# Kernel tuning notes

Measured on AMD Instinct MI355X. Metric: run time of the kernel, lower is better.

The kernel has to match this reference:

```python
import jax, jax.numpy as jnp
import numpy as np

B = 2048

def _conv(x, w, b, stride):
    y = jax.lax.conv_general_dilated(x, w, (stride, stride), 'VALID',
                                     dimension_numbers=('NCHW', 'OIHW', 'NCHW'))
    return y + b[None, :, None, None]

def _local_conv(x, w, b):
    # w: (Ho, Wo, Co, Ci, kh, kw), b: (Ho, Wo, Co); stride 1, valid
    Ho, Wo, Co, Ci, kh, kw = w.shape
    # patches: (B, Ci, kh*kw, Ho, Wo) -- sliding windows, small fixed loop over kernel taps
    patches = jnp.stack([x[:, :, i:i + Ho, j:j + Wo]
                         for i in range(kh) for j in range(kw)], axis=2)
    wf = w.reshape(Ho, Wo, Co, Ci, kh * kw)
    y = jnp.einsum('bcphw,hwocp->bohw', patches, wf)
    return y + jnp.transpose(b, (2, 0, 1))[None]

def setup_inputs() -> dict:
    key = jax.random.key(0)
    ks = jax.random.split(key, 18)
    s = 0.05
    inp = {
        'x': jax.random.normal(ks[0], (B, 5, 60, 60), dtype=jnp.float32),
        'info': jax.random.normal(ks[1], (B, 8), dtype=jnp.float32),
        'w1': jax.random.normal(ks[2], (32, 5, 3, 3), dtype=jnp.float32) * s,
        'b1': jnp.zeros((32,), dtype=jnp.float32),
        'w2a': jax.random.normal(ks[3], (64, 32, 3, 3), dtype=jnp.float32) * s,
        'b2a': jnp.zeros((64,), dtype=jnp.float32),
        'w2b': jax.random.normal(ks[4], (64, 64, 3, 3), dtype=jnp.float32) * s,
        'b2b': jnp.zeros((64,), dtype=jnp.float32),
        'lw3': jax.random.normal(ks[5], (9, 9, 64, 64, 5, 5), dtype=jnp.float32) * s,
        'lb3': jnp.zeros((9, 9, 64), dtype=jnp.float32),
        'lw4': jax.random.normal(ks[6], (5, 5, 64, 64, 5, 5), dtype=jnp.float32) * s,
        'lb4': jnp.zeros((5, 5, 64), dtype=jnp.float32),
        'lw5': jax.random.normal(ks[7], (3, 3, 64, 64, 3, 3), dtype=jnp.float32) * s,
        'lb5': jnp.zeros((3, 3, 64), dtype=jnp.float32),
        'hw': jax.random.normal(ks[8], (2, 584), dtype=jnp.float32) * s,
        'hb': jnp.zeros((2,), dtype=jnp.float32),
    }
    return inp

def reference(x, info, w1, b1, w2a, b2a, w2b, b2b, lw3, lb3, lw4, lb4, lw5, lb5, hw, hb):
    h = jnp.tanh(_conv(x, w1, b1, 2))            # (B,32,29,29)
    h = jnp.tanh(_conv(h, w2a, b2a, 1))          # (B,64,27,27)
    h = jnp.tanh(_conv(h, w2b, b2b, 2))          # (B,64,13,13)
    h = jnp.tanh(_local_conv(h, lw3, lb3))       # (B,64,9,9)
    h = jnp.tanh(_local_conv(h, lw4, lb4))       # (B,64,5,5)
    h = jnp.tanh(_local_conv(h, lw5, lb5))       # (B,64,3,3)
    h = h.reshape(h.shape[0], -1)                # (B,576)
    h = jnp.concatenate([h, info], axis=1)       # (B,584)
    logits = h @ hw.T + hb                       # (B,2)
    return jax.nn.softmax(logits, axis=1)
```

## Files before the change

### kernel.cpp

```cpp
#include <hip/hip_runtime.h>
#include <stdint.h>

#define THREADS 256

typedef short bf16x8 __attribute__((ext_vector_type(8)));
typedef float f32x4 __attribute__((ext_vector_type(4)));
typedef unsigned uint2_ __attribute__((ext_vector_type(2)));

#define GPTR(x) ((const __attribute__((address_space(1))) void*)(x))
#define LPTR(x) ((__attribute__((address_space(3))) void*)(x))

__device__ __forceinline__ unsigned short f2bf(float v) {
  unsigned u = __builtin_bit_cast(unsigned, v);
  u = (u + 0x7fff + ((u >> 16) & 1)) >> 16;
  return (unsigned short)u;
}
__device__ __forceinline__ float bf2f(unsigned short h) {
  return __builtin_bit_cast(float, (unsigned)h << 16);
}
__device__ __forceinline__ float fast_tanh(float x) {
  return 1.f - 2.f / (__expf(2.f * x) + 1.f);
}

__device__ __forceinline__ int xcd_swizzle(int wg, int nwg) {
  const int q = nwg >> 3, rr = nwg & 7;
  const int xcd = wg & 7, l = wg >> 3;
  return (xcd < rr ? xcd * (q + 1) : rr * (q + 1) + (xcd - rr) * q) + l;
}

__global__ void pack_w1t(const float* __restrict__ w1, float* __restrict__ w1t) {
  int idx = blockIdx.x * THREADS + threadIdx.x;
  if (idx >= 45 * 32) return;
  int t = idx >> 5, co = idx & 31;
  w1t[t * 32 + co] = w1[co * 45 + t];
}

__global__ void __launch_bounds__(256) conv1_direct(
    const float* __restrict__ x, const float* __restrict__ w1t,
    const float* __restrict__ bias, unsigned short* __restrict__ out, int Bc,
    int bstart) {
  constexpr int CI = 5, CO = 32, IH = 60, IW = 60, OH = 29, OW = 29;
  constexpr int RPB = 2, NRB = 15;

  __shared__ float xs[CI * 5 * 60];

  const int tid = threadIdx.x;
  const int b = blockIdx.x / NRB;
  const int qb = blockIdx.x % NRB;
  const int oh0 = qb * RPB;
  const int rows = min(RPB, OH - oh0);
  const int ih0 = oh0 * 2;
  const int ihn = rows * 2 + 1;

  const float* xp = x + (size_t)(bstart + b) * (CI * IH * IW);

  const int nf4 = CI * ihn * 15;
  for (int i = tid; i < nf4; i += 256) {
    int col = i % 15;
    int row = i / 15;
    int ci = row / ihn, r = row % ihn;
    ((float4*)xs)[row * 15 + col] = ((const float4*)xp)[(ci * IH + ih0 + r) * 15 + col];
  }
  __syncthreads();

  const int lane = tid & 63;
  const int wu = __builtin_amdgcn_readfirstlane(tid >> 6);
  if (lane >= rows * OW) return;
  const int r = lane / OW, c = lane % OW;
  const int base = (r * 2) * 60 + c * 2;
  const int cstr = ihn * 60;

  float acc[8];
#pragma unroll
  for (int j = 0; j < 8; j++) acc[j] = bias[wu * 8 + j];

#pragma unroll
  for (int ci = 0; ci < CI; ci++)
#pragma unroll
    for (int kh = 0; kh < 3; kh++)
#pragma unroll
      for (int kw = 0; kw < 3; kw++) {
        const float v = xs[ci * cstr + base + kh * 60 + kw];
        const float* wt = w1t + ((ci * 3 + kh) * 3 + kw) * 32 + wu * 8;
#pragma unroll
        for (int j = 0; j < 8; j++) acc[j] = fmaf(v, wt[j], acc[j]);
      }

  const int p = (oh0 + r) * OW + c;
  bf16x8 o;
#pragma unroll
  for (int j = 0; j < 8; j++) o[j] = (short)f2bf(fast_tanh(acc[j]));
  *(bf16x8*)(out + ((size_t)p * Bc + b) * CO + wu * 8) = o;
}

template <int CI, int KS>
__global__ void __launch_bounds__(THREADS) pack_w(const float* __restrict__ w,
                                                  unsigned short* __restrict__ wp,
                                                  int npos) {
  constexpr int K = CI * KS * KS;
  constexpr int S = K / 32;
  int idx = blockIdx.x * THREADS + threadIdx.x;
  int total = npos * S * 2048;
  if (idx >= total) return;
  int e = idx & 7;
  int lane = (idx >> 3) & 63;
  int mt = (idx >> 9) & 3;
  int rest = idx >> 11;
  int s = rest % S, pos = rest / S;
  int co = mt * 16 + (lane & 15);
  int k = s * 32 + (lane >> 4) * 8 + e;
  int tap = k / CI, ci = k % CI;
  int kh = tap / KS, kw = tap % KS;
  float v = w[((((size_t)pos * 64 + co) * CI + ci) * KS + kh) * KS + kw];
  wp[idx] = f2bf(v);
}

template <int CI, int IH, int IW, int OH, int OW, int KS, int ST, bool LOCAL, int BT>
__global__ void __launch_bounds__(256) conv_mfma(
    const unsigned short* __restrict__ X, const unsigned short* __restrict__ Wp,
    const float* __restrict__ bias, unsigned short* __restrict__ Y, int Bc,
    int bcsh) {
  constexpr int S = CI * KS * KS / 32;
  constexpr int NPOS = OH * OW;
  constexpr int NJ = BT / 64;
  constexpr int NB = BT / 64;
  constexpr int CISH = (CI == 64) ? 6 : 5;

  __shared__ unsigned short As[2][2048];
  __shared__ unsigned short Bs[2][BT * 32];

  const int tid = threadIdx.x;
  const int lane = tid & 63;
  const int wu = tid >> 6;
  const int n = lane & 15, g = lane >> 4;

  const int nbt = Bc / BT;
  int wg = xcd_swizzle(blockIdx.x, gridDim.x);
  int pos, btile;
  if (LOCAL) {
    btile = wg % nbt;
    pos = wg / nbt;
  } else {
    pos = wg % NPOS;
    btile = wg / NPOS;
  }
  const int oh = pos / OW, ow = pos % OW;
  const int b0 = btile * BT;

  const unsigned short* Wpp = Wp + (LOCAL ? (size_t)pos * (S * 2048) : 0);

  const int srow = tid >> 2;
  const int scol = (tid & 3) * 8;

  auto stage = [&](int s, int buf) {
    __builtin_amdgcn_global_load_lds(GPTR(Wpp + s * 2048 + tid * 8),
                                     LPTR(&As[buf][tid * 8]), 16, 0, 0);
    const int tap = (s * 32) / CI;
    const int ci0 = (s * 32) % CI;
    const int kh = tap / KS, kw = tap % KS;
    const int pin = (oh * ST + kh) * IW + (ow * ST + kw);
    const size_t base = ((size_t)pin << bcsh) + b0;
#pragma unroll
    for (int i = 0; i < NB; i++)
      __builtin_amdgcn_global_load_lds(
          GPTR(X + ((base + i * 64 + srow) << CISH) + ci0 + scol),
          LPTR(&Bs[buf][i * 2048 + tid * 8]), 16, 0, 0);
  };

  f32x4 acc[4][NJ] = {};

  stage(0, 0);
  int buf = 0;
  for (int s = 0; s < S; s++) {
    __syncthreads();
    if (s + 1 < S) stage(s + 1, buf ^ 1);

    bf16x8 bfr[NJ];
#pragma unroll
    for (int j = 0; j < NJ; j++) {
      const int local_b = wu * (NJ * 16) + j * 16 + n;
      bfr[j] = *(const bf16x8*)(&Bs[buf][local_b * 32 + g * 8]);
    }
    bf16x8 af[4];
#pragma unroll
    for (int mt = 0; mt < 4; mt++)
      af[mt] = *(const bf16x8*)(&As[buf][(mt * 64 + lane) * 8]);

#pragma unroll
    for (int mt = 0; mt < 4; mt++)
#pragma unroll
      for (int j = 0; j < NJ; j++)
        acc[mt][j] =
            __builtin_amdgcn_mfma_f32_16x16x32_bf16(af[mt], bfr[j], acc[mt][j], 0, 0, 0);
    buf ^= 1;
  }

#pragma unroll
  for (int mt = 0; mt < 4; mt++) {
#pragma unroll
    for (int j = 0; j < NJ; j++) {
      unsigned short o[4];
#pragma unroll
      for (int r = 0; r < 4; r++) {
        const int co = mt * 16 + g * 4 + r;
        o[r] = f2bf(fast_tanh(acc[mt][j][r] +
                              (LOCAL ? bias[pos * 64 + co] : bias[co])));
      }
      const int b = b0 + wu * (NJ * 16) + j * 16 + n;
      uint2_ pk;
      pk[0] = (unsigned)o[0] | ((unsigned)o[1] << 16);
      pk[1] = (unsigned)o[2] | ((unsigned)o[3] << 16);
      *(uint2_*)(Y + (((size_t)pos << bcsh) + b) * 64 + mt * 16 + g * 4) = pk;
    }
  }
}

__global__ void head_k(const unsigned short* __restrict__ h5,
                       const float* __restrict__ info, const float* __restrict__ hw,
                       const float* __restrict__ hb, float* __restrict__ out, int Bc,
                       int bstart) {
  int b = blockIdx.x * THREADS + threadIdx.x;
  if (b >= Bc) return;
  float l0 = hb[0], l1 = hb[1];
  for (int pos = 0; pos < 9; pos++) {
#pragma unroll
    for (int cb = 0; cb < 8; cb++) {
      bf16x8 v8 = *(const bf16x8*)(h5 + ((size_t)pos * Bc + b) * 64 + cb * 8);
#pragma unroll
      for (int j = 0; j < 8; j++) {
        float v = bf2f((unsigned short)v8[j]);
        int f = (cb * 8 + j) * 9 + pos;
        l0 = fmaf(v, hw[f], l0);
        l1 = fmaf(v, hw[584 + f], l1);
      }
    }
  }
#pragma unroll
  for (int k = 0; k < 8; k++) {
    float v = info[(size_t)(bstart + b) * 8 + k];
    l0 = fmaf(v, hw[576 + k], l0);
    l1 = fmaf(v, hw[584 + 576 + k], l1);
  }
  float m = fmaxf(l0, l1);
  float e0 = __expf(l0 - m), e1 = __expf(l1 - m);
  float s = e0 + e1;
  out[(size_t)(bstart + b) * 2 + 0] = e0 / s;
  out[(size_t)(bstart + b) * 2 + 1] = e1 / s;
}


static inline int ilog2i(int v) {
  int s = 0;
  while ((1 << s) < v) s++;
  return s;
}

extern "C" void kernel_launch(void* const* d_in, const int* in_sizes, int n_in,
                              void* d_out, int out_size, void* d_ws, size_t ws_size,
                              hipStream_t stream) {
  const float* x = (const float*)d_in[0];
  const float* info = (const float*)d_in[1];
  const float* w1 = (const float*)d_in[2];
  const float* b1 = (const float*)d_in[3];
  const float* w2a = (const float*)d_in[4];
  const float* b2a = (const float*)d_in[5];
  const float* w2b = (const float*)d_in[6];
  const float* b2b = (const float*)d_in[7];
  const float* lw3 = (const float*)d_in[8];
  const float* lb3 = (const float*)d_in[9];
  const float* lw4 = (const float*)d_in[10];
  const float* lb4 = (const float*)d_in[11];
  const float* lw5 = (const float*)d_in[12];
  const float* lb5 = (const float*)d_in[13];
  const float* hw = (const float*)d_in[14];
  const float* hb = (const float*)d_in[15];
  float* out = (float*)d_out;

  const int B = in_sizes[0] / 18000;

  const size_t SZ2A = 9ull * 2048, SZ2B = 18ull * 2048, SZ3 = 81ull * 50 * 2048,
               SZ4 = 25ull * 50 * 2048, SZ5 = 9ull * 18 * 2048;
  unsigned short* wp2a = (unsigned short*)d_ws;
  unsigned short* wp2b = wp2a + SZ2A;
  unsigned short* wp3 = wp2b + SZ2B;
  unsigned short* wp4 = wp3 + SZ3;
  unsigned short* wp5 = wp4 + SZ4;
  size_t wp_bytes = (SZ2A + SZ2B + SZ3 + SZ4 + SZ5) * 2;
  wp_bytes = (wp_bytes + 255) & ~(size_t)255;
  float* w1t = (float*)((char*)d_ws + wp_bytes);
  size_t w1t_bytes = ((45 * 32 * 4) + 255) & ~(size_t)255;

  const size_t PSA = 53824, PSB = 93312;
  const size_t per_sample = PSA + PSB;
  int Bc = B;
  while (Bc > 256 && wp_bytes + w1t_bytes + (size_t)Bc * per_sample + 4096 > ws_size)
    Bc >>= 1;
  const int bcsh = ilog2i(Bc);

  char* base = (char*)d_ws + wp_bytes + w1t_bytes;
  unsigned short* bufA = (unsigned short*)base;
  unsigned short* bufB = (unsigned short*)(base + (size_t)Bc * PSA);

  hipLaunchKernelGGL(pack_w1t, dim3(6), dim3(THREADS), 0, stream, w1, w1t);
  hipLaunchKernelGGL((pack_w<32, 3>), dim3((SZ2A + 255) / 256), dim3(THREADS), 0, stream,
                     w2a, wp2a, 1);
  hipLaunchKernelGGL((pack_w<64, 3>), dim3((SZ2B + 255) / 256), dim3(THREADS), 0, stream,
                     w2b, wp2b, 1);
  hipLaunchKernelGGL((pack_w<64, 5>), dim3((SZ3 + 255) / 256), dim3(THREADS), 0, stream,
                     lw3, wp3, 81);
  hipLaunchKernelGGL((pack_w<64, 5>), dim3((SZ4 + 255) / 256), dim3(THREADS), 0, stream,
                     lw4, wp4, 25);
  hipLaunchKernelGGL((pack_w<64, 3>), dim3((SZ5 + 255) / 256), dim3(THREADS), 0, stream,
                     lw5, wp5, 9);

  const int nchunks = B / Bc;
  for (int c = 0; c < nchunks; c++) {
    const int bstart = c * Bc;

    hipLaunchKernelGGL(conv1_direct, dim3(Bc * 15), dim3(256), 0, stream, x, w1t, b1,
                       bufA, Bc, bstart);
    hipLaunchKernelGGL((conv_mfma<32, 29, 29, 27, 27, 3, 1, false, 128>),
                       dim3(729 * (Bc / 128)), dim3(256), 0, stream, bufA, wp2a, b2a,
                       bufB, Bc, bcsh);
    hipLaunchKernelGGL((conv_mfma<64, 27, 27, 13, 13, 3, 2, false, 128>),
                       dim3(169 * (Bc / 128)), dim3(256), 0, stream, bufB, wp2b, b2b,
                       bufA, Bc, bcsh);
    hipLaunchKernelGGL((conv_mfma<64, 13, 13, 9, 9, 5, 1, true, 128>),
                       dim3(81 * (Bc / 128)), dim3(256), 0, stream, bufA, wp3, lb3, bufB,
                       Bc, bcsh);
    hipLaunchKernelGGL((conv_mfma<64, 9, 9, 5, 5, 5, 1, true, 128>),
                       dim3(25 * (Bc / 128)), dim3(256), 0, stream, bufB, wp4, lb4, bufA,
                       Bc, bcsh);
    hipLaunchKernelGGL((conv_mfma<64, 5, 5, 3, 3, 3, 1, true, 64>),
                       dim3(9 * (Bc / 64)), dim3(256), 0, stream, bufA, wp5, lb5, bufB,
                       Bc, bcsh);
    hipLaunchKernelGGL(head_k, dim3((Bc + THREADS - 1) / THREADS), dim3(THREADS), 0,
                       stream, bufB, info, hw, hb, out, Bc, bstart);
  }
}
```

Measured before the change: 548.8 us.

## Stage two K-slices per barrier and XOR-swizzle B tile in LDS

Each pipeline step of the MFMA convolution kernel now loads SK=2 K-slices of 32 into a double buffer, which halves the number of __syncthreads per reduction and gives the MFMAs more work between barriers. The B-tile LDS layout is also XOR-swizzled so the bf16x8 fragment reads avoid bank conflicts. LDS use per block doubles, which may lower occupancy. The swizzle is applied the same way on the write side and the read side.

```diff
diff --git a/kernel.cpp b/kernel.cpp
--- a/kernel.cpp
+++ b/kernel.cpp
@@ -115,7 +115,8 @@
   wp[idx] = f2bf(v);
 }
 
-template <int CI, int IH, int IW, int OH, int OW, int KS, int ST, bool LOCAL, int BT>
+template <int CI, int IH, int IW, int OH, int OW, int KS, int ST, bool LOCAL, int BT,
+          int SK>
 __global__ void __launch_bounds__(256) conv_mfma(
     const unsigned short* __restrict__ X, const unsigned short* __restrict__ Wp,
     const float* __restrict__ bias, unsigned short* __restrict__ Y, int Bc,
@@ -125,9 +126,13 @@
   constexpr int NJ = BT / 64;
   constexpr int NB = BT / 64;
   constexpr int CISH = (CI == 64) ? 6 : 5;
-
-  __shared__ unsigned short As[2][2048];
-  __shared__ unsigned short Bs[2][BT * 32];
+  constexpr int NFULL = S / SK;
+  constexpr int TAIL = S % SK;
+  constexpr int NSTEP = NFULL + (TAIL ? 1 : 0);
+  constexpr int BSLICE = BT * 32;
+
+  __shared__ unsigned short As[2][SK * 2048];
+  __shared__ unsigned short Bs[2][SK * BSLICE];
 
   const int tid = threadIdx.x;
   const int lane = tid & 63;
@@ -149,49 +154,62 @@
 
   const unsigned short* Wpp = Wp + (LOCAL ? (size_t)pos * (S * 2048) : 0);
 
-  const int srow = tid >> 2;
-  const int scol = (tid & 3) * 8;
-
-  auto stage = [&](int s, int buf) {
-    __builtin_amdgcn_global_load_lds(GPTR(Wpp + s * 2048 + tid * 8),
-                                     LPTR(&As[buf][tid * 8]), 16, 0, 0);
-    const int tap = (s * 32) / CI;
-    const int ci0 = (s * 32) % CI;
-    const int kh = tap / KS, kw = tap % KS;
-    const int pin = (oh * ST + kh) * IW + (ow * ST + kw);
-    const size_t base = ((size_t)pin << bcsh) + b0;
-#pragma unroll
-    for (int i = 0; i < NB; i++)
-      __builtin_amdgcn_global_load_lds(
-          GPTR(X + ((base + i * 64 + srow) << CISH) + ci0 + scol),
-          LPTR(&Bs[buf][i * 2048 + tid * 8]), 16, 0, 0);
+  auto stage = [&](int s0, int cnt, int buf) {
+#pragma unroll
+    for (int q = 0; q < SK; q++) {
+      if (q >= cnt) break;
+      const int s = s0 + q;
+      __builtin_amdgcn_global_load_lds(GPTR(Wpp + s * 2048 + tid * 8),
+                                       LPTR(&As[buf][q * 2048 + tid * 8]), 16, 0, 0);
+      const int tap = (s * 32) / CI;
+      const int ci0 = (s * 32) % CI;
+      const int kh = tap / KS, kw = tap % KS;
+      const int pin = (oh * ST + kh) * IW + (ow * ST + kw);
+      const size_t base = ((size_t)pin << bcsh) + b0;
+#pragma unroll
+      for (int i = 0; i < NB; i++) {
+        const int d = i * 256 + tid;
+        const int u = d ^ ((d >> 3) & 7);
+        const int bt = u >> 2, gg = u & 3;
+        __builtin_amdgcn_global_load_lds(
+            GPTR(X + ((base + bt) << CISH) + ci0 + gg * 8),
+            LPTR(&Bs[buf][q * BSLICE + d * 8]), 16, 0, 0);
+      }
+    }
   };
 
   f32x4 acc[4][NJ] = {};
 
-  stage(0, 0);
+  stage(0, SK < S ? SK : S, 0);
   int buf = 0;
-  for (int s = 0; s < S; s++) {
+  for (int t = 0; t < NSTEP; t++) {
     __syncthreads();
-    if (s + 1 < S) stage(s + 1, buf ^ 1);
-
-    bf16x8 bfr[NJ];
-#pragma unroll
-    for (int j = 0; j < NJ; j++) {
-      const int local_b = wu * (NJ * 16) + j * 16 + n;
-      bfr[j] = *(const bf16x8*)(&Bs[buf][local_b * 32 + g * 8]);
+    const int nxt = t + 1;
+    if (nxt < NSTEP) stage(nxt * SK, (nxt < NFULL) ? SK : TAIL, buf ^ 1);
+
+    const int cnt = (t < NFULL) ? SK : TAIL;
+#pragma unroll
+    for (int q = 0; q < SK; q++) {
+      if (q >= cnt) break;
+      bf16x8 bfr[NJ];
+#pragma unroll
+      for (int j = 0; j < NJ; j++) {
+        const int ub = ((wu * (NJ * 16) + j * 16 + n) << 2) | g;
+        const int p = ub ^ ((ub >> 3) & 7);
+        bfr[j] = *(const bf16x8*)(&Bs[buf][q * BSLICE + p * 8]);
+      }
+      bf16x8 af[4];
+#pragma unroll
+      for (int mt = 0; mt < 4; mt++)
+        af[mt] = *(const bf16x8*)(&As[buf][q * 2048 + (mt * 64 + lane) * 8]);
+
+#pragma unroll
+      for (int mt = 0; mt < 4; mt++)
+#pragma unroll
+        for (int j = 0; j < NJ; j++)
+          acc[mt][j] = __builtin_amdgcn_mfma_f32_16x16x32_bf16(af[mt], bfr[j],
+                                                               acc[mt][j], 0, 0, 0);
     }
-    bf16x8 af[4];
-#pragma unroll
-    for (int mt = 0; mt < 4; mt++)
-      af[mt] = *(const bf16x8*)(&As[buf][(mt * 64 + lane) * 8]);
-
-#pragma unroll
-    for (int mt = 0; mt < 4; mt++)
-#pragma unroll
-      for (int j = 0; j < NJ; j++)
-        acc[mt][j] =
-            __builtin_amdgcn_mfma_f32_16x16x32_bf16(af[mt], bfr[j], acc[mt][j], 0, 0, 0);
     buf ^= 1;
   }
 
@@ -319,19 +337,19 @@
 
     hipLaunchKernelGGL(conv1_direct, dim3(Bc * 15), dim3(256), 0, stream, x, w1t, b1,
                        bufA, Bc, bstart);
-    hipLaunchKernelGGL((conv_mfma<32, 29, 29, 27, 27, 3, 1, false, 128>),
+    hipLaunchKernelGGL((conv_mfma<32, 29, 29, 27, 27, 3, 1, false, 128, 2>),
                        dim3(729 * (Bc / 128)), dim3(256), 0, stream, bufA, wp2a, b2a,
                        bufB, Bc, bcsh);
-    hipLaunchKernelGGL((conv_mfma<64, 27, 27, 13, 13, 3, 2, false, 128>),
+    hipLaunchKernelGGL((conv_mfma<64, 27, 27, 13, 13, 3, 2, false, 128, 2>),
                        dim3(169 * (Bc / 128)), dim3(256), 0, stream, bufB, wp2b, b2b,
                        bufA, Bc, bcsh);
-    hipLaunchKernelGGL((conv_mfma<64, 13, 13, 9, 9, 5, 1, true, 128>),
+    hipLaunchKernelGGL((conv_mfma<64, 13, 13, 9, 9, 5, 1, true, 128, 2>),
                        dim3(81 * (Bc / 128)), dim3(256), 0, stream, bufA, wp3, lb3, bufB,
                        Bc, bcsh);
-    hipLaunchKernelGGL((conv_mfma<64, 9, 9, 5, 5, 5, 1, true, 128>),
+    hipLaunchKernelGGL((conv_mfma<64, 9, 9, 5, 5, 5, 1, true, 128, 2>),
                        dim3(25 * (Bc / 128)), dim3(256), 0, stream, bufB, wp4, lb4, bufA,
                        Bc, bcsh);
-    hipLaunchKernelGGL((conv_mfma<64, 5, 5, 3, 3, 3, 1, true, 64>),
+    hipLaunchKernelGGL((conv_mfma<64, 5, 5, 3, 3, 3, 1, true, 64, 2>),
                        dim3(9 * (Bc / 64)), dim3(256), 0, stream, bufA, wp5, lb5, bufB,
                        Bc, bcsh);
     hipLaunchKernelGGL(head_k, dim3((Bc + THREADS - 1) / THREADS), dim3(THREADS), 0,
```

Measured after the change: 548.5 us. Within noise of the previous version (-0.1%).
